# Optimization experiments

Measured on AMD Instinct MI355X. Metric: run time of the kernel, lower is better.

The kernel has to match this reference:

```python
import jax, jax.numpy as jnp
import numpy as np

T, B, N, C = 4, 16, 256, 512
H = 8
HID = 4 * C
TAU = 2.0
EPS = 1e-5
SCALE = 0.125

@jax.custom_vjp
def spike_fn(x):
    return (x >= 0.0).astype(x.dtype)

def _spike_fwd(x):
    return spike_fn(x), x

def _spike_bwd(x, g):
    alpha = 4.0  # spikingjelly sigmoid surrogate default
    s = jax.nn.sigmoid(alpha * x)
    return (g * alpha * s * (1.0 - s),)

spike_fn.defvjp(_spike_fwd, _spike_bwd)

def lif(x_seq, v_th=1.0):
    # Multi-step LIF: v += (x - v)/tau (decay_input, v_reset=0), hard reset, detach_reset
    def step(v, xt):
        v = v + (xt - v) / TAU
        s = spike_fn(v - v_th)
        v = v * (1.0 - jax.lax.stop_gradient(s))
        return v, s
    _, out = jax.lax.scan(step, jnp.zeros_like(x_seq[0]), x_seq)
    return out

def lin_bn(x2d, w, b, g, beta):
    # Linear then BatchNorm1d (training mode, per-channel stats over all rows).
    # BN on (TB, Cout, N) over (batch, N) == BN on flattened (TB*N, Cout) over axis 0.
    y = x2d @ w.T + b
    mu = jnp.mean(y, axis=0)
    var = jnp.var(y, axis=0)
    return g * (y - mu) * jax.lax.rsqrt(var + EPS) + beta

def setup_inputs() -> dict:
    key = jax.random.key(0)
    ks = jax.random.split(key, 10)
    d = {
        "x": jax.random.normal(ks[0], (T, B, N, C), jnp.float32),
        "s_x": jax.random.normal(ks[1], (T, B, N, C), jnp.float32),
    }
    def lin(k, cout, cin):
        return jax.random.normal(k, (cout, cin), jnp.float32) * 0.02
    d["qw"] = lin(ks[2], C, C); d["qb"] = jnp.zeros((C,), jnp.float32)
    d["qg"] = jnp.ones((C,), jnp.float32); d["qbeta"] = jnp.zeros((C,), jnp.float32)
    d["kw"] = lin(ks[3], C, C); d["kb"] = jnp.zeros((C,), jnp.float32)
    d["kg"] = jnp.ones((C,), jnp.float32); d["kbeta"] = jnp.zeros((C,), jnp.float32)
    d["vw"] = lin(ks[4], C, C); d["vb"] = jnp.zeros((C,), jnp.float32)
    d["vg"] = jnp.ones((C,), jnp.float32); d["vbeta"] = jnp.zeros((C,), jnp.float32)
    d["pw"] = lin(ks[5], C, C); d["pb"] = jnp.zeros((C,), jnp.float32)
    d["pg"] = jnp.ones((C,), jnp.float32); d["pbeta"] = jnp.zeros((C,), jnp.float32)
    d["f1w"] = lin(ks[6], HID, C); d["f1b"] = jnp.zeros((HID,), jnp.float32)
    d["f1g"] = jnp.ones((HID,), jnp.float32); d["f1beta"] = jnp.zeros((HID,), jnp.float32)
    d["f2w"] = lin(ks[7], C, HID); d["f2b"] = jnp.zeros((C,), jnp.float32)
    d["f2g"] = jnp.ones((C,), jnp.float32); d["f2beta"] = jnp.zeros((C,), jnp.float32)
    return d

def _block(x, s_x, qw, qb, qg, qbeta, kw, kb, kg, kbeta, vw, vb, vg, vbeta,
           pw, pb, pg, pbeta, f1w, f1b, f1g, f1beta, f2w, f2b, f2g, f2beta):
    Dh = C // H
    xf = x.reshape(T * B * N, C)
    # SSA (s_x is unused in the source forward)
    q = lif(lin_bn(xf, qw, qb, qg, qbeta).reshape(T, B, N, C))
    k = lif(lin_bn(xf, kw, kb, kg, kbeta).reshape(T, B, N, C))
    v = lin_bn(xf, vw, vb, vg, vbeta).reshape(T, B, N, C)  # v has no LIF in source
    q = q.reshape(T, B, N, H, Dh).transpose(0, 1, 3, 2, 4)  # tbhnd
    k = k.reshape(T, B, N, H, Dh).transpose(0, 1, 3, 2, 4)
    v = v.reshape(T, B, N, H, Dh).transpose(0, 1, 3, 2, 4)
    attn = jnp.einsum('tbhnd,tbhmd->tbhnm', q, k) * SCALE  # no softmax
    o = jnp.einsum('tbhnm,tbhmd->tbhnd', attn, v)
    o = o.transpose(0, 1, 3, 2, 4).reshape(T * B * N, C)
    o = lin_bn(o, pw, pb, pg, pbeta).reshape(T, B, N, C)
    x = x + o
    # MLP
    xf2 = x.reshape(T * B * N, C)
    h = lif(lin_bn(xf2, f1w, f1b, f1g, f1beta).reshape(T, B, N, HID))
    m = lif(lin_bn(h.reshape(T * B * N, HID), f2w, f2b, f2g, f2beta).reshape(T, B, N, C))
    return x + m

def reference(x, s_x, qw, qb, qg, qbeta, kw, kb, kg, kbeta, vw, vb, vg, vbeta,
              pw, pb, pg, pbeta, f1w, f1b, f1g, f1beta, f2w, f2b, f2g, f2beta):
    return _block(x, s_x, qw, qb, qg, qbeta, kw, kb, kg, kbeta, vw, vb, vg, vbeta,
                  pw, pb, pg, pbeta, f1w, f1b, f1g, f1beta, f2w, f2b, f2g, f2beta)
```

## Files before the change

kernel.cpp:

```cpp
#include <hip/hip_runtime.h>
#include <cstdint>

#define T_ 4
#define B_ 16
#define N_ 256
#define C_ 512
#define H_ 8
#define HID_ 2048
#define M_ (T_*B_*N_)
#define BNP_ (B_*N_)

__global__ __launch_bounds__(256, 2)
void gemm_f32_t128(const float* __restrict__ A, const float* __restrict__ W,
                   const float* __restrict__ bias, float* __restrict__ Y,
                   int Nc, int K) {
  __shared__ float As[2][16][132];
  __shared__ float Ws[2][16][132];
  const int tid  = threadIdx.x;
  const int row0 = blockIdx.y * 128;
  const int col0 = blockIdx.x * 128;
  const int tx = tid & 15, ty = tid >> 4;
  const int ar = tid >> 2;
  const int ac = (tid & 3) << 2;

  float acc[8][8];
  #pragma unroll
  for (int i = 0; i < 8; ++i)
    #pragma unroll
    for (int j = 0; j < 8; ++j) acc[i][j] = 0.f;

  const float* Ap0 = A + (size_t)(row0 + ar) * K + ac;
  const float* Ap1 = A + (size_t)(row0 + ar + 64) * K + ac;
  const float* Wp0 = W + (size_t)(col0 + ar) * K + ac;
  const float* Wp1 = W + (size_t)(col0 + ar + 64) * K + ac;

  float4 pa0 = *(const float4*)Ap0;
  float4 pa1 = *(const float4*)Ap1;
  float4 pw0 = *(const float4*)Wp0;
  float4 pw1 = *(const float4*)Wp1;
  As[0][ac+0][ar] = pa0.x; As[0][ac+1][ar] = pa0.y; As[0][ac+2][ar] = pa0.z; As[0][ac+3][ar] = pa0.w;
  As[0][ac+0][ar+64] = pa1.x; As[0][ac+1][ar+64] = pa1.y; As[0][ac+2][ar+64] = pa1.z; As[0][ac+3][ar+64] = pa1.w;
  Ws[0][ac+0][ar] = pw0.x; Ws[0][ac+1][ar] = pw0.y; Ws[0][ac+2][ar] = pw0.z; Ws[0][ac+3][ar] = pw0.w;
  Ws[0][ac+0][ar+64] = pw1.x; Ws[0][ac+1][ar+64] = pw1.y; Ws[0][ac+2][ar+64] = pw1.z; Ws[0][ac+3][ar+64] = pw1.w;
  __syncthreads();

  int buf = 0;
  for (int k0 = 0; k0 < K; k0 += 16) {
    const bool last = (k0 + 16 >= K);
    if (!last) {
      pa0 = *(const float4*)(Ap0 + k0 + 16);
      pa1 = *(const float4*)(Ap1 + k0 + 16);
      pw0 = *(const float4*)(Wp0 + k0 + 16);
      pw1 = *(const float4*)(Wp1 + k0 + 16);
    }
    #pragma unroll
    for (int kk = 0; kk < 16; ++kk) {
      float a[8], b[8];
      *(float4*)&a[0] = *(const float4*)&As[buf][kk][ty*4];
      *(float4*)&a[4] = *(const float4*)&As[buf][kk][64 + ty*4];
      *(float4*)&b[0] = *(const float4*)&Ws[buf][kk][tx*4];
      *(float4*)&b[4] = *(const float4*)&Ws[buf][kk][64 + tx*4];
      #pragma unroll
      for (int i = 0; i < 8; ++i)
        #pragma unroll
        for (int j = 0; j < 8; ++j)
          acc[i][j] = fmaf(a[i], b[j], acc[i][j]);
    }
    if (!last) {
      int nb = buf ^ 1;
      As[nb][ac+0][ar] = pa0.x; As[nb][ac+1][ar] = pa0.y; As[nb][ac+2][ar] = pa0.z; As[nb][ac+3][ar] = pa0.w;
      As[nb][ac+0][ar+64] = pa1.x; As[nb][ac+1][ar+64] = pa1.y; As[nb][ac+2][ar+64] = pa1.z; As[nb][ac+3][ar+64] = pa1.w;
      Ws[nb][ac+0][ar] = pw0.x; Ws[nb][ac+1][ar] = pw0.y; Ws[nb][ac+2][ar] = pw0.z; Ws[nb][ac+3][ar] = pw0.w;
      Ws[nb][ac+0][ar+64] = pw1.x; Ws[nb][ac+1][ar+64] = pw1.y; Ws[nb][ac+2][ar+64] = pw1.z; Ws[nb][ac+3][ar+64] = pw1.w;
      __syncthreads();
      buf = nb;
    }
  }

  #pragma unroll
  for (int ih = 0; ih < 2; ++ih)
    #pragma unroll
    for (int i = 0; i < 4; ++i) {
      size_t r = (size_t)(row0 + ih*64 + ty*4 + i);
      #pragma unroll
      for (int jh = 0; jh < 2; ++jh) {
        int c = col0 + jh*64 + tx*4;
        float4 o4;
        o4.x = acc[ih*4+i][jh*4+0] + bias[c+0];
        o4.y = acc[ih*4+i][jh*4+1] + bias[c+1];
        o4.z = acc[ih*4+i][jh*4+2] + bias[c+2];
        o4.w = acc[ih*4+i][jh*4+3] + bias[c+3];
        *(float4*)(Y + r * Nc + c) = o4;
      }
    }
}

__global__ __launch_bounds__(256, 2)
void gemm_f32_f2sparse(const unsigned long long* __restrict__ hmask,
                       const float* __restrict__ W, const float* __restrict__ bias,
                       float* __restrict__ Y) {
  __shared__ float Ws[2][64][132];
  __shared__ unsigned long long Ms[2][64];
  const int tid  = threadIdx.x;
  const int row0 = blockIdx.y * 64;
  const int col0 = blockIdx.x * 128;
  const int lane = tid & 63, wv = tid >> 6;
  const int sc  = tid >> 1;
  const int skq = (tid & 1) * 32;

  float acc[16][2];
  #pragma unroll
  for (int i = 0; i < 16; ++i) { acc[i][0] = 0.f; acc[i][1] = 0.f; }

  const float* Wp = W + (size_t)(col0 + sc) * 2048 + skq;

  #pragma unroll
  for (int i = 0; i < 8; ++i) {
    float4 w4 = *(const float4*)(Wp + 4*i);
    Ws[0][skq+4*i+0][sc] = w4.x; Ws[0][skq+4*i+1][sc] = w4.y;
    Ws[0][skq+4*i+2][sc] = w4.z; Ws[0][skq+4*i+3][sc] = w4.w;
  }
  if (tid < 64) Ms[0][tid] = hmask[(size_t)(row0 + tid) * 32];
  __syncthreads();

  int buf = 0;
  for (int ch = 0; ch < 32; ++ch) {
    const bool last = (ch == 31);
    float4 pw[8];
    unsigned long long pm = 0;
    if (!last) {
      #pragma unroll
      for (int i = 0; i < 8; ++i) pw[i] = *(const float4*)(Wp + (ch+1)*64 + 4*i);
      if (tid < 64) pm = hmask[(size_t)(row0 + tid) * 32 + ch + 1];
    }
    #pragma unroll
    for (int ri = 0; ri < 16; ++ri) {
      unsigned long long m = Ms[buf][wv*16 + ri];
      while (m) {
        int k = __builtin_ctzll(m);
        m &= m - 1;
        float2 b2 = *(const float2*)&Ws[buf][k][lane*2];
        acc[ri][0] = acc[ri][0] + b2.x;
        acc[ri][1] = acc[ri][1] + b2.y;
      }
    }
    if (!last) {
      int nb = buf ^ 1;
      #pragma unroll
      for (int i = 0; i < 8; ++i) {
        Ws[nb][skq+4*i+0][sc] = pw[i].x; Ws[nb][skq+4*i+1][sc] = pw[i].y;
        Ws[nb][skq+4*i+2][sc] = pw[i].z; Ws[nb][skq+4*i+3][sc] = pw[i].w;
      }
      if (tid < 64) Ms[nb][tid] = pm;
      __syncthreads();
      buf = nb;
    }
  }

  #pragma unroll
  for (int ri = 0; ri < 16; ++ri) {
    size_t r = (size_t)(row0 + wv*16 + ri);
    int c = col0 + lane*2;
    float2 o2;
    o2.x = acc[ri][0] + bias[c+0];
    o2.y = acc[ri][1] + bias[c+1];
    *(float2*)(Y + r * 512 + c) = o2;
  }
}

__global__ __launch_bounds__(256, 2)
void gemm_f32_qk(const float* __restrict__ A,
                 const float* __restrict__ Wq, const float* __restrict__ bq,
                 const float* __restrict__ Wk, const float* __restrict__ bk,
                 float* __restrict__ Yq, float* __restrict__ Yk,
                 int Nc, int K) {
  __shared__ float As[2][16][68];
  __shared__ float Wqs[2][16][132];
  __shared__ float Wks[2][16][132];
  const int tid  = threadIdx.x;
  const int row0 = blockIdx.y * 64;
  const int col0 = blockIdx.x * 128;
  const int tx = tid & 15, ty = tid >> 4;
  const int ar = tid >> 2;
  const int ac = (tid & 3) << 2;

  float accq[4][8], acck[4][8];
  #pragma unroll
  for (int i = 0; i < 4; ++i)
    #pragma unroll
    for (int j = 0; j < 8; ++j) { accq[i][j] = 0.f; acck[i][j] = 0.f; }

  const float* Ap   = A  + (size_t)(row0 + ar) * K + ac;
  const float* Wqp0 = Wq + (size_t)(col0 + ar) * K + ac;
  const float* Wqp1 = Wq + (size_t)(col0 + ar + 64) * K + ac;
  const float* Wkp0 = Wk + (size_t)(col0 + ar) * K + ac;
  const float* Wkp1 = Wk + (size_t)(col0 + ar + 64) * K + ac;

  float4 pa  = *(const float4*)Ap;
  float4 pq0 = *(const float4*)Wqp0;
  float4 pq1 = *(const float4*)Wqp1;
  float4 pk0 = *(const float4*)Wkp0;
  float4 pk1 = *(const float4*)Wkp1;
  As[0][ac+0][ar] = pa.x; As[0][ac+1][ar] = pa.y; As[0][ac+2][ar] = pa.z; As[0][ac+3][ar] = pa.w;
  Wqs[0][ac+0][ar] = pq0.x; Wqs[0][ac+1][ar] = pq0.y; Wqs[0][ac+2][ar] = pq0.z; Wqs[0][ac+3][ar] = pq0.w;
  Wqs[0][ac+0][ar+64] = pq1.x; Wqs[0][ac+1][ar+64] = pq1.y; Wqs[0][ac+2][ar+64] = pq1.z; Wqs[0][ac+3][ar+64] = pq1.w;
  Wks[0][ac+0][ar] = pk0.x; Wks[0][ac+1][ar] = pk0.y; Wks[0][ac+2][ar] = pk0.z; Wks[0][ac+3][ar] = pk0.w;
  Wks[0][ac+0][ar+64] = pk1.x; Wks[0][ac+1][ar+64] = pk1.y; Wks[0][ac+2][ar+64] = pk1.z; Wks[0][ac+3][ar+64] = pk1.w;
  __syncthreads();

  int buf = 0;
  for (int k0 = 0; k0 < K; k0 += 16) {
    const bool last = (k0 + 16 >= K);
    if (!last) {
      pa  = *(const float4*)(Ap   + k0 + 16);
      pq0 = *(const float4*)(Wqp0 + k0 + 16);
      pq1 = *(const float4*)(Wqp1 + k0 + 16);
      pk0 = *(const float4*)(Wkp0 + k0 + 16);
      pk1 = *(const float4*)(Wkp1 + k0 + 16);
    }
    #pragma unroll
    for (int kk = 0; kk < 16; ++kk) {
      float4 av = *(const float4*)&As[buf][kk][ty*4];
      float a[4] = {av.x, av.y, av.z, av.w};
      float b[8];
      *(float4*)&b[0] = *(const float4*)&Wqs[buf][kk][tx*4];
      *(float4*)&b[4] = *(const float4*)&Wqs[buf][kk][64 + tx*4];
      #pragma unroll
      for (int i = 0; i < 4; ++i)
        #pragma unroll
        for (int j = 0; j < 8; ++j)
          accq[i][j] = fmaf(a[i], b[j], accq[i][j]);
      *(float4*)&b[0] = *(const float4*)&Wks[buf][kk][tx*4];
      *(float4*)&b[4] = *(const float4*)&Wks[buf][kk][64 + tx*4];
      #pragma unroll
      for (int i = 0; i < 4; ++i)
        #pragma unroll
        for (int j = 0; j < 8; ++j)
          acck[i][j] = fmaf(a[i], b[j], acck[i][j]);
    }
    if (!last) {
      int nb = buf ^ 1;
      As[nb][ac+0][ar] = pa.x; As[nb][ac+1][ar] = pa.y; As[nb][ac+2][ar] = pa.z; As[nb][ac+3][ar] = pa.w;
      Wqs[nb][ac+0][ar] = pq0.x; Wqs[nb][ac+1][ar] = pq0.y; Wqs[nb][ac+2][ar] = pq0.z; Wqs[nb][ac+3][ar] = pq0.w;
      Wqs[nb][ac+0][ar+64] = pq1.x; Wqs[nb][ac+1][ar+64] = pq1.y; Wqs[nb][ac+2][ar+64] = pq1.z; Wqs[nb][ac+3][ar+64] = pq1.w;
      Wks[nb][ac+0][ar] = pk0.x; Wks[nb][ac+1][ar] = pk0.y; Wks[nb][ac+2][ar] = pk0.z; Wks[nb][ac+3][ar] = pk0.w;
      Wks[nb][ac+0][ar+64] = pk1.x; Wks[nb][ac+1][ar+64] = pk1.y; Wks[nb][ac+2][ar+64] = pk1.z; Wks[nb][ac+3][ar+64] = pk1.w;
      __syncthreads();
      buf = nb;
    }
  }

  #pragma unroll
  for (int i = 0; i < 4; ++i) {
    size_t r = (size_t)(row0 + ty*4 + i);
    #pragma unroll
    for (int jh = 0; jh < 2; ++jh) {
      int c = col0 + jh*64 + tx*4;
      float4 oq, ok;
      oq.x = accq[i][jh*4+0] + bq[c+0];
      oq.y = accq[i][jh*4+1] + bq[c+1];
      oq.z = accq[i][jh*4+2] + bq[c+2];
      oq.w = accq[i][jh*4+3] + bq[c+3];
      *(float4*)(Yq + r * Nc + c) = oq;
      ok.x = acck[i][jh*4+0] + bk[c+0];
      ok.y = acck[i][jh*4+1] + bk[c+1];
      ok.z = acck[i][jh*4+2] + bk[c+2];
      ok.w = acck[i][jh*4+3] + bk[c+3];
      *(float4*)(Yk + r * Nc + c) = ok;
    }
  }
}

__global__ __launch_bounds__(256, 2)
void gemm_f64_v3(const float* __restrict__ A, const float* __restrict__ W,
                 const float* __restrict__ bias, float* __restrict__ Y,
                 int Nc, int K) {
  __shared__ double As[2][16][68];
  __shared__ double Ws[2][16][132];
  const int tid  = threadIdx.x;
  const int row0 = blockIdx.y * 64;
  const int col0 = blockIdx.x * 128;
  const int tx = tid & 15, ty = tid >> 4;
  const int lr = tid >> 2;
  const int lk = (tid & 3) << 2;

  double acc[4][8];
  #pragma unroll
  for (int i = 0; i < 4; ++i)
    #pragma unroll
    for (int j = 0; j < 8; ++j) acc[i][j] = 0.0;

  const float* Ap  = A + (size_t)(row0 + lr) * K + lk;
  const float* Wp0 = W + (size_t)(col0 + lr) * K + lk;
  const float* Wp1 = W + (size_t)(col0 + lr + 64) * K + lk;

  float4 pa  = *(const float4*)Ap;
  float4 pw0 = *(const float4*)Wp0;
  float4 pw1 = *(const float4*)Wp1;
  As[0][lk+0][lr] = (double)pa.x; As[0][lk+1][lr] = (double)pa.y;
  As[0][lk+2][lr] = (double)pa.z; As[0][lk+3][lr] = (double)pa.w;
  Ws[0][lk+0][lr] = (double)pw0.x; Ws[0][lk+1][lr] = (double)pw0.y;
  Ws[0][lk+2][lr] = (double)pw0.z; Ws[0][lk+3][lr] = (double)pw0.w;
  Ws[0][lk+0][lr+64] = (double)pw1.x; Ws[0][lk+1][lr+64] = (double)pw1.y;
  Ws[0][lk+2][lr+64] = (double)pw1.z; Ws[0][lk+3][lr+64] = (double)pw1.w;
  __syncthreads();

  int buf = 0;
  for (int k0 = 0; k0 < K; k0 += 16) {
    const bool last = (k0 + 16 >= K);
    if (!last) {
      pa  = *(const float4*)(Ap  + k0 + 16);
      pw0 = *(const float4*)(Wp0 + k0 + 16);
      pw1 = *(const float4*)(Wp1 + k0 + 16);
    }
    #pragma unroll
    for (int kk = 0; kk < 16; ++kk) {
      double a[4], b[8];
      *(double2*)&a[0] = *(const double2*)&As[buf][kk][ty*4];
      *(double2*)&a[2] = *(const double2*)&As[buf][kk][ty*4+2];
      *(double2*)&b[0] = *(const double2*)&Ws[buf][kk][tx*2];
      *(double2*)&b[2] = *(const double2*)&Ws[buf][kk][32 + tx*2];
      *(double2*)&b[4] = *(const double2*)&Ws[buf][kk][64 + tx*2];
      *(double2*)&b[6] = *(const double2*)&Ws[buf][kk][96 + tx*2];
      #pragma unroll
      for (int i = 0; i < 4; ++i)
        #pragma unroll
        for (int j = 0; j < 8; ++j)
          acc[i][j] = fma(a[i], b[j], acc[i][j]);
    }
    if (!last) {
      int nb = buf ^ 1;
      As[nb][lk+0][lr] = (double)pa.x; As[nb][lk+1][lr] = (double)pa.y;
      As[nb][lk+2][lr] = (double)pa.z; As[nb][lk+3][lr] = (double)pa.w;
      Ws[nb][lk+0][lr] = (double)pw0.x; Ws[nb][lk+1][lr] = (double)pw0.y;
      Ws[nb][lk+2][lr] = (double)pw0.z; Ws[nb][lk+3][lr] = (double)pw0.w;
      Ws[nb][lk+0][lr+64] = (double)pw1.x; Ws[nb][lk+1][lr+64] = (double)pw1.y;
      Ws[nb][lk+2][lr+64] = (double)pw1.z; Ws[nb][lk+3][lr+64] = (double)pw1.w;
      __syncthreads();
      buf = nb;
    }
  }

  #pragma unroll
  for (int i = 0; i < 4; ++i) {
    size_t r = (size_t)(row0 + ty*4 + i);
    #pragma unroll
    for (int g = 0; g < 4; ++g) {
      int c = col0 + g*32 + tx*2;
      float2 o2;
      o2.x = (float)(acc[i][g*2+0] + (double)bias[c+0]);
      o2.y = (float)(acc[i][g*2+1] + (double)bias[c+1]);
      *(float2*)(Y + r * Nc + c) = o2;
    }
  }
}

__global__ __launch_bounds__(256)
void col_stats_partial(const float* __restrict__ Y, int Nc,
                       float* __restrict__ psum, float* __restrict__ psq) {
  const int r0 = blockIdx.x * 32;
  for (int c = threadIdx.x; c < Nc; c += 256) {
    float s = 0.f, q = 0.f;
    const float* p = Y + (size_t)r0 * Nc + c;
    for (int r = 0; r < 32; ++r) {
      float v = p[(size_t)r * Nc];
      s += v;
      q = fmaf(v, v, q);
    }
    psum[(size_t)blockIdx.x * Nc + c] = s;
    psq [(size_t)blockIdx.x * Nc + c] = q;
  }
}

__global__ void col_stats_final(const float* __restrict__ psum, const float* __restrict__ psq,
                                int Nc, const float* __restrict__ g, const float* __restrict__ beta,
                                float* __restrict__ chp) {
  int c = blockIdx.x * blockDim.x + threadIdx.x;
  if (c >= Nc) return;
  double s = 0.0, q = 0.0;
  for (int p = 0; p < 512; ++p) {
    s += (double)psum[(size_t)p * Nc + c];
    q += (double)psq [(size_t)p * Nc + c];
  }
  double mean = s / (double)M_;
  double var  = q / (double)M_ - mean * mean;
  float alpha = g[c] / sqrtf((float)var + 1e-5f);
  chp[2*c]   = alpha;
  chp[2*c+1] = fmaf(-(float)mean, alpha, beta[c]);
}

__global__ void col_stats_final_f64(const float* __restrict__ psum, const float* __restrict__ psq,
                                    int Nc, const float* __restrict__ g, const float* __restrict__ beta,
                                    double* __restrict__ chpd) {
  int c = blockIdx.x * blockDim.x + threadIdx.x;
  if (c >= Nc) return;
  double s = 0.0, q = 0.0;
  for (int p = 0; p < 512; ++p) {
    s += (double)psum[(size_t)p * Nc + c];
    q += (double)psq [(size_t)p * Nc + c];
  }
  double mean = s / (double)M_;
  double var  = q / (double)M_ - mean * mean;
  double alpha = (double)g[c] / sqrt(var + 1e-5);
  chpd[2*c]   = alpha;
  chpd[2*c+1] = (double)beta[c] - mean * alpha;
}

__global__ __launch_bounds__(256)
void bnlif_mask(const float* __restrict__ Y, const float* __restrict__ chp,
                unsigned long long* __restrict__ mask) {
  int lane = threadIdx.x & 63;
  int u  = blockIdx.x * 4 + (threadIdx.x >> 6);
  int bn = u >> 3, cg = u & 7;
  int c  = cg * 64 + lane;
  float alpha = chp[2*c], bb = chp[2*c+1];
  float v = 0.f;
  #pragma unroll
  for (int t = 0; t < 4; ++t) {
    float y  = Y[((size_t)(t * BNP_ + bn)) * C_ + c];
    float uu = fmaf(y, alpha, bb);
    v = v + (uu - v) * 0.5f;
    bool sp = (v >= 1.0f);
    unsigned long long m = __ballot(sp);
    if (sp) v = 0.f;
    if (lane == 0) mask[((size_t)(t * BNP_ + bn)) * H_ + cg] = m;
  }
}

__global__ void bn_apply_f64(const float* __restrict__ Y, const double* __restrict__ chpd,
                             float* __restrict__ out) {
  const long total4 = (long)M_ * C_ / 4;
  for (long i = (long)blockIdx.x * blockDim.x + threadIdx.x; i < total4;
       i += (long)gridDim.x * blockDim.x) {
    int c4 = (int)(i & (C_/4 - 1)) * 4;
    float4 y = ((const float4*)Y)[i];
    float4 r;
    r.x = (float)fma((double)y.x, chpd[2*(c4+0)], chpd[2*(c4+0)+1]);
    r.y = (float)fma((double)y.y, chpd[2*(c4+1)], chpd[2*(c4+1)+1]);
    r.z = (float)fma((double)y.z, chpd[2*(c4+2)], chpd[2*(c4+2)+1]);
    r.w = (float)fma((double)y.w, chpd[2*(c4+3)], chpd[2*(c4+3)+1]);
    ((float4*)out)[i] = r;
  }
}

__global__ void bn_residual_f64(const float* __restrict__ Y, const double* __restrict__ chpd,
                                const float* __restrict__ x, float* __restrict__ out) {
  const long total4 = (long)M_ * C_ / 4;
  for (long i = (long)blockIdx.x * blockDim.x + threadIdx.x; i < total4;
       i += (long)gridDim.x * blockDim.x) {
    int c4 = (int)(i & (C_/4 - 1)) * 4;
    float4 y = ((const float4*)Y)[i];
    float4 xv = ((const float4*)x)[i];
    float4 r;
    r.x = (float)((double)xv.x + fma((double)y.x, chpd[2*(c4+0)], chpd[2*(c4+0)+1]));
    r.y = (float)((double)xv.y + fma((double)y.y, chpd[2*(c4+1)], chpd[2*(c4+1)+1]));
    r.z = (float)((double)xv.z + fma((double)y.z, chpd[2*(c4+2)], chpd[2*(c4+2)+1]));
    r.w = (float)((double)xv.w + fma((double)y.w, chpd[2*(c4+3)], chpd[2*(c4+3)+1]));
    ((float4*)out)[i] = r;
  }
}

__global__ __launch_bounds__(256)
void bnlif_hmask(const float* __restrict__ Y, const float* __restrict__ chp,
                 unsigned long long* __restrict__ hmask) {
  int c  = blockIdx.x * 256 + threadIdx.x;
  int bn = blockIdx.y;
  int lane = threadIdx.x & 63;
  int word = blockIdx.x * 4 + (threadIdx.x >> 6);
  float alpha = chp[2*c], bb = chp[2*c+1];
  float v = 0.f;
  #pragma unroll
  for (int t = 0; t < 4; ++t) {
    size_t row = (size_t)(t * BNP_ + bn);
    float uu = fmaf(Y[row * HID_ + c], alpha, bb);
    v = v + (uu - v) * 0.5f;
    bool sp = (v >= 1.f);
    unsigned long long m = __ballot(sp);
    if (sp) v = 0.f;
    if (lane == 0) hmask[row * 32 + word] = m;
  }
}

__global__ __launch_bounds__(256)
void bnlif_final(const float* __restrict__ Y, const float* __restrict__ chp,
                 const float* __restrict__ xo, float* __restrict__ out) {
  int c  = blockIdx.x * 256 + threadIdx.x;
  int bn = blockIdx.y;
  float alpha = chp[2*c], bb = chp[2*c+1];
  float v = 0.f;
  #pragma unroll
  for (int t = 0; t < 4; ++t) {
    size_t idx = ((size_t)(t * BNP_ + bn)) * C_ + c;
    float uu = fmaf(Y[idx], alpha, bb);
    v = v + (uu - v) * 0.5f;
    bool sp = (v >= 1.f);
    out[idx] = xo[idx] + (sp ? 1.f : 0.f);
    if (sp) v = 0.f;
  }
}

__global__ __launch_bounds__(256)
void attn_kernel_f64(const unsigned long long* __restrict__ qmask,
                     const unsigned long long* __restrict__ kmask,
                     const float* __restrict__ v, float* __restrict__ o) {
  __shared__ unsigned long long km[256];
  __shared__ float vt[256][64];
  int rb  = blockIdx.x & 3;
  int tbh = blockIdx.x >> 2;
  int h   = tbh & 7, tb = tbh >> 3;
  int tid = threadIdx.x;

  km[tid] = kmask[(size_t)(tb * 256 + tid) * H_ + h];
  const float* vbase = v + (size_t)tb * 256 * C_ + h * 64;
  #pragma unroll
  for (int i = 0; i < 16; ++i) {
    int f = i * 256 + tid;
    int r = f >> 4, c4 = f & 15;
    *(float4*)&vt[r][c4 * 4] = *(const float4*)(vbase + (size_t)r * C_ + c4 * 4);
  }
  int lane = tid & 63, w = tid >> 6;
  int nr = lane & 15, dg = lane >> 4;
  int n  = rb * 64 + w * 16 + nr;
  unsigned long long qm = qmask[(size_t)(tb * 256 + n) * H_ + h];
  __syncthreads();

  double acc[16];
  #pragma unroll
  for (int j = 0; j < 16; ++j) acc[j] = 0.0;

  for (int m = 0; m < 256; ++m) {
    double s = (double)__popcll(qm & km[m]) * 0.125;
    #pragma unroll
    for (int j = 0; j < 4; ++j) {
      float4 vv = *(const float4*)&vt[m][dg * 16 + j * 4];
      acc[j*4+0] = fma(s, (double)vv.x, acc[j*4+0]);
      acc[j*4+1] = fma(s, (double)vv.y, acc[j*4+1]);
      acc[j*4+2] = fma(s, (double)vv.z, acc[j*4+2]);
      acc[j*4+3] = fma(s, (double)vv.w, acc[j*4+3]);
    }
  }
  float* orow = o + (size_t)(tb * 256 + n) * C_ + h * 64 + dg * 16;
  #pragma unroll
  for (int j = 0; j < 4; ++j)
    *(float4*)(orow + j * 4) = make_float4((float)acc[j*4], (float)acc[j*4+1],
                                           (float)acc[j*4+2], (float)acc[j*4+3]);
}

extern "C" void kernel_launch(void* const* d_in, const int* in_sizes, int n_in,
                              void* d_out, int out_size, void* d_ws, size_t ws_size,
                              hipStream_t stream) {
  const float* x    = (const float*)d_in[0];
  const float* qw   = (const float*)d_in[2];
  const float* qb   = (const float*)d_in[3];
  const float* qg   = (const float*)d_in[4];
  const float* qbe  = (const float*)d_in[5];
  const float* kw   = (const float*)d_in[6];
  const float* kb   = (const float*)d_in[7];
  const float* kg   = (const float*)d_in[8];
  const float* kbe  = (const float*)d_in[9];
  const float* vw   = (const float*)d_in[10];
  const float* vb   = (const float*)d_in[11];
  const float* vg   = (const float*)d_in[12];
  const float* vbe  = (const float*)d_in[13];
  const float* pw   = (const float*)d_in[14];
  const float* pb   = (const float*)d_in[15];
  const float* pg   = (const float*)d_in[16];
  const float* pbe  = (const float*)d_in[17];
  const float* f1w  = (const float*)d_in[18];
  const float* f1b  = (const float*)d_in[19];
  const float* f1g  = (const float*)d_in[20];
  const float* f1be = (const float*)d_in[21];
  const float* f2w  = (const float*)d_in[22];
  const float* f2b  = (const float*)d_in[23];
  const float* f2g  = (const float*)d_in[24];
  const float* f2be = (const float*)d_in[25];

  char* ws = (char*)d_ws;
  float* bufY = (float*)(ws);
  float* bufK = bufY + 8388608;
  float* bufV = (float*)(ws + 134217728ull);
  float* bufO = (float*)(ws + 167772160ull);
  unsigned long long* qmask = (unsigned long long*)(ws + 201326592ull);
  unsigned long long* kmask = (unsigned long long*)(ws + 202375168ull);
  float* psum = (float*)(ws + 203423744ull);
  float* psq  = (float*)(ws + 207618048ull);
  float* chp  = (float*)(ws + 211812352ull);
  double* chpd = (double*)(ws + 211828736ull);
  unsigned long long* hmask = (unsigned long long*)bufV;

  float* out = (float*)d_out;

  gemm_f32_qk<<<dim3(4,256), 256, 0, stream>>>(x, qw, qb, kw, kb, bufY, bufK, C_, C_);
  col_stats_partial<<<512, 256, 0, stream>>>(bufY, C_, psum, psq);
  col_stats_final<<<2, 256, 0, stream>>>(psum, psq, C_, qg, qbe, chp);
  bnlif_mask<<<8192, 256, 0, stream>>>(bufY, chp, qmask);
  col_stats_partial<<<512, 256, 0, stream>>>(bufK, C_, psum, psq);
  col_stats_final<<<2, 256, 0, stream>>>(psum, psq, C_, kg, kbe, chp);
  bnlif_mask<<<8192, 256, 0, stream>>>(bufK, chp, kmask);
  gemm_f64_v3<<<dim3(4,256), 256, 0, stream>>>(x, vw, vb, bufY, C_, C_);
  col_stats_partial<<<512, 256, 0, stream>>>(bufY, C_, psum, psq);
  col_stats_final_f64<<<2, 256, 0, stream>>>(psum, psq, C_, vg, vbe, chpd);
  bn_apply_f64<<<2048, 256, 0, stream>>>(bufY, chpd, bufV);
  attn_kernel_f64<<<2048, 256, 0, stream>>>(qmask, kmask, bufV, bufO);
  gemm_f64_v3<<<dim3(4,256), 256, 0, stream>>>(bufO, pw, pb, bufY, C_, C_);
  col_stats_partial<<<512, 256, 0, stream>>>(bufY, C_, psum, psq);
  col_stats_final_f64<<<2, 256, 0, stream>>>(psum, psq, C_, pg, pbe, chpd);
  bn_residual_f64<<<2048, 256, 0, stream>>>(bufY, chpd, x, bufO);
  gemm_f32_t128<<<dim3(16,128), 256, 0, stream>>>(bufO, f1w, f1b, bufY, HID_, C_);
  col_stats_partial<<<512, 256, 0, stream>>>(bufY, HID_, psum, psq);
  col_stats_final<<<8, 256, 0, stream>>>(psum, psq, HID_, f1g, f1be, chp);
  bnlif_hmask<<<dim3(8,4096), 256, 0, stream>>>(bufY, chp, hmask);
  gemm_f32_f2sparse<<<dim3(4,256), 256, 0, stream>>>(hmask, f2w, f2b, bufY);
  col_stats_partial<<<512, 256, 0, stream>>>(bufY, C_, psum, psq);
  col_stats_final<<<2, 256, 0, stream>>>(psum, psq, C_, f2g, f2be, chp);
  bnlif_final<<<dim3(2,4096), 256, 0, stream>>>(bufY, chp, bufO, out);
}
```

Measured before the change: 1.810 ms.

## Fuse V batchnorm into attention, shrink f64 GEMM smem, make FFN2 mask GEMM dense

```diff
diff --git a/kernel.cpp b/kernel.cpp
--- a/kernel.cpp
+++ b/kernel.cpp
@@ -96,9 +96,9 @@
 }
 
 __global__ __launch_bounds__(256, 2)
-void gemm_f32_f2sparse(const unsigned long long* __restrict__ hmask,
-                       const float* __restrict__ W, const float* __restrict__ bias,
-                       float* __restrict__ Y) {
+void gemm_f32_f2mask(const unsigned long long* __restrict__ hmask,
+                     const float* __restrict__ W, const float* __restrict__ bias,
+                     float* __restrict__ Y) {
   __shared__ float Ws[2][64][132];
   __shared__ unsigned long long Ms[2][64];
   const int tid  = threadIdx.x;
@@ -133,15 +133,25 @@
       for (int i = 0; i < 8; ++i) pw[i] = *(const float4*)(Wp + (ch+1)*64 + 4*i);
       if (tid < 64) pm = hmask[(size_t)(row0 + tid) * 32 + ch + 1];
     }
+    unsigned int mlo[16], mhi[16];
     #pragma unroll
     for (int ri = 0; ri < 16; ++ri) {
       unsigned long long m = Ms[buf][wv*16 + ri];
-      while (m) {
-        int k = __builtin_ctzll(m);
-        m &= m - 1;
-        float2 b2 = *(const float2*)&Ws[buf][k][lane*2];
-        acc[ri][0] = acc[ri][0] + b2.x;
-        acc[ri][1] = acc[ri][1] + b2.y;
+      mlo[ri] = (unsigned int)m;
+      mhi[ri] = (unsigned int)(m >> 32);
+    }
+    #pragma unroll
+    for (int half = 0; half < 2; ++half) {
+      #pragma unroll 8
+      for (int k = 0; k < 32; ++k) {
+        float2 w = *(const float2*)&Ws[buf][half*32 + k][lane*2];
+        #pragma unroll
+        for (int ri = 0; ri < 16; ++ri) {
+          unsigned int bit = (half ? mhi[ri] : mlo[ri]) >> k;
+          float a = (float)(bit & 1u);
+          acc[ri][0] = fmaf(a, w.x, acc[ri][0]);
+          acc[ri][1] = fmaf(a, w.y, acc[ri][1]);
+        }
       }
     }
     if (!last) {
@@ -272,17 +282,17 @@
 }
 
 __global__ __launch_bounds__(256, 2)
-void gemm_f64_v3(const float* __restrict__ A, const float* __restrict__ W,
+void gemm_f64_v4(const float* __restrict__ A, const float* __restrict__ W,
                  const float* __restrict__ bias, float* __restrict__ Y,
                  int Nc, int K) {
-  __shared__ double As[2][16][68];
-  __shared__ double Ws[2][16][132];
+  __shared__ float As[2][16][68];
+  __shared__ float Ws[2][16][132];
   const int tid  = threadIdx.x;
   const int row0 = blockIdx.y * 64;
   const int col0 = blockIdx.x * 128;
   const int tx = tid & 15, ty = tid >> 4;
-  const int lr = tid >> 2;
-  const int lk = (tid & 3) << 2;
+  const int ar = tid >> 2;
+  const int ac = (tid & 3) << 2;
 
   double acc[4][8];
   #pragma unroll
@@ -290,19 +300,16 @@
     #pragma unroll
     for (int j = 0; j < 8; ++j) acc[i][j] = 0.0;
 
-  const float* Ap  = A + (size_t)(row0 + lr) * K + lk;
-  const float* Wp0 = W + (size_t)(col0 + lr) * K + lk;
-  const float* Wp1 = W + (size_t)(col0 + lr + 64) * K + lk;
+  const float* Ap  = A + (size_t)(row0 + ar) * K + ac;
+  const float* Wp0 = W + (size_t)(col0 + ar) * K + ac;
+  const float* Wp1 = W + (size_t)(col0 + ar + 64) * K + ac;
 
   float4 pa  = *(const float4*)Ap;
   float4 pw0 = *(const float4*)Wp0;
   float4 pw1 = *(const float4*)Wp1;
-  As[0][lk+0][lr] = (double)pa.x; As[0][lk+1][lr] = (double)pa.y;
-  As[0][lk+2][lr] = (double)pa.z; As[0][lk+3][lr] = (double)pa.w;
-  Ws[0][lk+0][lr] = (double)pw0.x; Ws[0][lk+1][lr] = (double)pw0.y;
-  Ws[0][lk+2][lr] = (double)pw0.z; Ws[0][lk+3][lr] = (double)pw0.w;
-  Ws[0][lk+0][lr+64] = (double)pw1.x; Ws[0][lk+1][lr+64] = (double)pw1.y;
-  Ws[0][lk+2][lr+64] = (double)pw1.z; Ws[0][lk+3][lr+64] = (double)pw1.w;
+  As[0][ac+0][ar] = pa.x; As[0][ac+1][ar] = pa.y; As[0][ac+2][ar] = pa.z; As[0][ac+3][ar] = pa.w;
+  Ws[0][ac+0][ar] = pw0.x; Ws[0][ac+1][ar] = pw0.y; Ws[0][ac+2][ar] = pw0.z; Ws[0][ac+3][ar] = pw0.w;
+  Ws[0][ac+0][ar+64] = pw1.x; Ws[0][ac+1][ar+64] = pw1.y; Ws[0][ac+2][ar+64] = pw1.z; Ws[0][ac+3][ar+64] = pw1.w;
   __syncthreads();
 
   int buf = 0;
@@ -315,13 +322,12 @@
     }
     #pragma unroll
     for (int kk = 0; kk < 16; ++kk) {
-      double a[4], b[8];
-      *(double2*)&a[0] = *(const double2*)&As[buf][kk][ty*4];
-      *(double2*)&a[2] = *(const double2*)&As[buf][kk][ty*4+2];
-      *(double2*)&b[0] = *(const double2*)&Ws[buf][kk][tx*2];
-      *(double2*)&b[2] = *(const double2*)&Ws[buf][kk][32 + tx*2];
-      *(double2*)&b[4] = *(const double2*)&Ws[buf][kk][64 + tx*2];
-      *(double2*)&b[6] = *(const double2*)&Ws[buf][kk][96 + tx*2];
+      float4 av  = *(const float4*)&As[buf][kk][ty*4];
+      float4 bv0 = *(const float4*)&Ws[buf][kk][tx*4];
+      float4 bv1 = *(const float4*)&Ws[buf][kk][64 + tx*4];
+      double a[4] = {(double)av.x, (double)av.y, (double)av.z, (double)av.w};
+      double b[8] = {(double)bv0.x, (double)bv0.y, (double)bv0.z, (double)bv0.w,
+                     (double)bv1.x, (double)bv1.y, (double)bv1.z, (double)bv1.w};
       #pragma unroll
       for (int i = 0; i < 4; ++i)
         #pragma unroll
@@ -330,12 +336,9 @@
     }
     if (!last) {
       int nb = buf ^ 1;
-      As[nb][lk+0][lr] = (double)pa.x; As[nb][lk+1][lr] = (double)pa.y;
-      As[nb][lk+2][lr] = (double)pa.z; As[nb][lk+3][lr] = (double)pa.w;
-      Ws[nb][lk+0][lr] = (double)pw0.x; Ws[nb][lk+1][lr] = (double)pw0.y;
-      Ws[nb][lk+2][lr] = (double)pw0.z; Ws[nb][lk+3][lr] = (double)pw0.w;
-      Ws[nb][lk+0][lr+64] = (double)pw1.x; Ws[nb][lk+1][lr+64] = (double)pw1.y;
-      Ws[nb][lk+2][lr+64] = (double)pw1.z; Ws[nb][lk+3][lr+64] = (double)pw1.w;
+      As[nb][ac+0][ar] = pa.x; As[nb][ac+1][ar] = pa.y; As[nb][ac+2][ar] = pa.z; As[nb][ac+3][ar] = pa.w;
+      Ws[nb][ac+0][ar] = pw0.x; Ws[nb][ac+1][ar] = pw0.y; Ws[nb][ac+2][ar] = pw0.z; Ws[nb][ac+3][ar] = pw0.w;
+      Ws[nb][ac+0][ar+64] = pw1.x; Ws[nb][ac+1][ar+64] = pw1.y; Ws[nb][ac+2][ar+64] = pw1.z; Ws[nb][ac+3][ar+64] = pw1.w;
       __syncthreads();
       buf = nb;
     }
@@ -345,12 +348,14 @@
   for (int i = 0; i < 4; ++i) {
     size_t r = (size_t)(row0 + ty*4 + i);
     #pragma unroll
-    for (int g = 0; g < 4; ++g) {
-      int c = col0 + g*32 + tx*2;
-      float2 o2;
-      o2.x = (float)(acc[i][g*2+0] + (double)bias[c+0]);
-      o2.y = (float)(acc[i][g*2+1] + (double)bias[c+1]);
-      *(float2*)(Y + r * Nc + c) = o2;
+    for (int jh = 0; jh < 2; ++jh) {
+      int c = col0 + jh*64 + tx*4;
+      float4 o4;
+      o4.x = (float)(acc[i][jh*4+0] + (double)bias[c+0]);
+      o4.y = (float)(acc[i][jh*4+1] + (double)bias[c+1]);
+      o4.z = (float)(acc[i][jh*4+2] + (double)bias[c+2]);
+      o4.w = (float)(acc[i][jh*4+3] + (double)bias[c+3]);
+      *(float4*)(Y + r * Nc + c) = o4;
     }
   }
 }
@@ -424,22 +429,6 @@
     unsigned long long m = __ballot(sp);
     if (sp) v = 0.f;
     if (lane == 0) mask[((size_t)(t * BNP_ + bn)) * H_ + cg] = m;
-  }
-}
-
-__global__ void bn_apply_f64(const float* __restrict__ Y, const double* __restrict__ chpd,
-                             float* __restrict__ out) {
-  const long total4 = (long)M_ * C_ / 4;
-  for (long i = (long)blockIdx.x * blockDim.x + threadIdx.x; i < total4;
-       i += (long)gridDim.x * blockDim.x) {
-    int c4 = (int)(i & (C_/4 - 1)) * 4;
-    float4 y = ((const float4*)Y)[i];
-    float4 r;
-    r.x = (float)fma((double)y.x, chpd[2*(c4+0)], chpd[2*(c4+0)+1]);
-    r.y = (float)fma((double)y.y, chpd[2*(c4+1)], chpd[2*(c4+1)+1]);
-    r.z = (float)fma((double)y.z, chpd[2*(c4+2)], chpd[2*(c4+2)+1]);
-    r.w = (float)fma((double)y.w, chpd[2*(c4+3)], chpd[2*(c4+3)+1]);
-    ((float4*)out)[i] = r;
   }
 }
 
@@ -502,7 +491,8 @@
 __global__ __launch_bounds__(256)
 void attn_kernel_f64(const unsigned long long* __restrict__ qmask,
                      const unsigned long long* __restrict__ kmask,
-                     const float* __restrict__ v, float* __restrict__ o) {
+                     const float* __restrict__ vraw, const double* __restrict__ chpd,
+                     float* __restrict__ o) {
   __shared__ unsigned long long km[256];
   __shared__ float vt[256][64];
   int rb  = blockIdx.x & 3;
@@ -511,12 +501,17 @@
   int tid = threadIdx.x;
 
   km[tid] = kmask[(size_t)(tb * 256 + tid) * H_ + h];
-  const float* vbase = v + (size_t)tb * 256 * C_ + h * 64;
+  const float* vbase = vraw + (size_t)tb * 256 * C_ + h * 64;
   #pragma unroll
   for (int i = 0; i < 16; ++i) {
     int f = i * 256 + tid;
     int r = f >> 4, c4 = f & 15;
-    *(float4*)&vt[r][c4 * 4] = *(const float4*)(vbase + (size_t)r * C_ + c4 * 4);
+    float4 y = *(const float4*)(vbase + (size_t)r * C_ + c4 * 4);
+    int ch = h * 64 + c4 * 4;
+    vt[r][c4*4+0] = (float)fma((double)y.x, chpd[2*(ch+0)], chpd[2*(ch+0)+1]);
+    vt[r][c4*4+1] = (float)fma((double)y.y, chpd[2*(ch+1)], chpd[2*(ch+1)+1]);
+    vt[r][c4*4+2] = (float)fma((double)y.z, chpd[2*(ch+2)], chpd[2*(ch+2)+1]);
+    vt[r][c4*4+3] = (float)fma((double)y.w, chpd[2*(ch+3)], chpd[2*(ch+3)+1]);
   }
   int lane = tid & 63, w = tid >> 6;
   int nr = lane & 15, dg = lane >> 4;
@@ -597,12 +592,11 @@
   col_stats_partial<<<512, 256, 0, stream>>>(bufK, C_, psum, psq);
   col_stats_final<<<2, 256, 0, stream>>>(psum, psq, C_, kg, kbe, chp);
   bnlif_mask<<<8192, 256, 0, stream>>>(bufK, chp, kmask);
-  gemm_f64_v3<<<dim3(4,256), 256, 0, stream>>>(x, vw, vb, bufY, C_, C_);
+  gemm_f64_v4<<<dim3(4,256), 256, 0, stream>>>(x, vw, vb, bufY, C_, C_);
   col_stats_partial<<<512, 256, 0, stream>>>(bufY, C_, psum, psq);
   col_stats_final_f64<<<2, 256, 0, stream>>>(psum, psq, C_, vg, vbe, chpd);
-  bn_apply_f64<<<2048, 256, 0, stream>>>(bufY, chpd, bufV);
-  attn_kernel_f64<<<2048, 256, 0, stream>>>(qmask, kmask, bufV, bufO);
-  gemm_f64_v3<<<dim3(4,256), 256, 0, stream>>>(bufO, pw, pb, bufY, C_, C_);
+  attn_kernel_f64<<<2048, 256, 0, stream>>>(qmask, kmask, bufY, chpd, bufO);
+  gemm_f64_v4<<<dim3(4,256), 256, 0, stream>>>(bufO, pw, pb, bufY, C_, C_);
   col_stats_partial<<<512, 256, 0, stream>>>(bufY, C_, psum, psq);
   col_stats_final_f64<<<2, 256, 0, stream>>>(psum, psq, C_, pg, pbe, chpd);
   bn_residual_f64<<<2048, 256, 0, stream>>>(bufY, chpd, x, bufO);
@@ -610,7 +604,7 @@
   col_stats_partial<<<512, 256, 0, stream>>>(bufY, HID_, psum, psq);
   col_stats_final<<<8, 256, 0, stream>>>(psum, psq, HID_, f1g, f1be, chp);
   bnlif_hmask<<<dim3(8,4096), 256, 0, stream>>>(bufY, chp, hmask);
-  gemm_f32_f2sparse<<<dim3(4,256), 256, 0, stream>>>(hmask, f2w, f2b, bufY);
+  gemm_f32_f2mask<<<dim3(4,256), 256, 0, stream>>>(hmask, f2w, f2b, bufY);
   col_stats_partial<<<512, 256, 0, stream>>>(bufY, C_, psum, psq);
   col_stats_final<<<2, 256, 0, stream>>>(psum, psq, C_, f2g, f2be, chp);
   bnlif_final<<<dim3(2,4096), 256, 0, stream>>>(bufY, chp, bufO, out);
```

Measured after the change: 2.619 ms. 44.7% more time.
